# Optimization experiments

Hardware: AMD Instinct MI355X
Metric: run time of the kernel (lower is better)

The kernel has to match this reference:

```python
import jax, jax.numpy as jnp
import numpy as np

N = 50000
E = 800000
IN_DIM, HID, OUT = 128, 256, 256


def setup_inputs() -> dict:
    key = jax.random.key(0)
    ks = jax.random.split(key, 6)
    x = jax.random.normal(ks[0], (N, IN_DIM), dtype=jnp.float32)
    edge_index = jax.random.randint(ks[1], (2, E), 0, N, dtype=jnp.int64)
    W1 = jax.random.normal(ks[2], (IN_DIM, HID), dtype=jnp.float32) / np.sqrt(IN_DIM)
    b1 = jnp.zeros((HID,), dtype=jnp.float32)
    W2 = jax.random.normal(ks[3], (HID, OUT), dtype=jnp.float32) / np.sqrt(HID)
    b2 = jnp.zeros((OUT,), dtype=jnp.float32)
    return {"x": x, "edge_index": edge_index, "W1": W1, "b1": b1, "W2": W2, "b2": b2}


def _gcn_conv(x, edge_index, W, b):
    """PyG GCNConv: add self-loops, symmetric deg^-1/2 norm, linear, scatter-add, bias."""
    n = x.shape[0]
    loops = jnp.arange(n, dtype=edge_index.dtype)
    src = jnp.concatenate([edge_index[0], loops])  # [E+N]
    dst = jnp.concatenate([edge_index[1], loops])  # [E+N]
    deg = jax.ops.segment_sum(jnp.ones(src.shape[0], dtype=x.dtype), dst, num_segments=n)
    dinv = jnp.where(deg > 0, jax.lax.rsqrt(deg), jnp.zeros_like(deg))
    norm = dinv[src] * dinv[dst]  # [E+N]
    h = x @ W  # [N, out] small GEMM before gather (PyG order)
    msg = h[src] * norm[:, None]  # [E+N, out] -- dominant memory traffic
    out = jax.ops.segment_sum(msg, dst, num_segments=n)
    return out + b


def reference(x, edge_index, W1, b1, W2, b2):
    h = jax.nn.relu(_gcn_conv(x, edge_index, W1, b1))
    # dropout is identity in eval mode
    out = _gcn_conv(h, edge_index, W2, b2)
    # F.normalize(p=2, dim=-1, eps=1e-12)
    nrm = jnp.maximum(jnp.linalg.norm(out, axis=-1, keepdims=True), 1e-12)
    return out / nrm
```

## Files before the change

kernel.cpp:

```cpp
#include <hip/hip_runtime.h>
#include <hip/hip_bf16.h>


#define NNODE 50000
#define FDIM 256
#define SCAN_CHUNK 2048

typedef __attribute__((ext_vector_type(8))) short short8;
typedef __attribute__((ext_vector_type(4))) float f32x4;

__device__ __forceinline__ float bf2f(unsigned short u) {
    union { unsigned int i; float f; } c;
    c.i = ((unsigned int)u) << 16;
    return c.f;
}
__device__ __forceinline__ unsigned short f2bf(float f) {
    __hip_bfloat16 h = __float2bfloat16(f);
    return *reinterpret_cast<unsigned short*>(&h);
}

__global__ void count_kernel(const int* __restrict__ ei, int* __restrict__ counts, int E) {
    int e = blockIdx.x * blockDim.x + threadIdx.x;
    if (e < E) atomicAdd(&counts[ei[E + e]], 1);
}

__global__ __launch_bounds__(256) void scan_part1(const int* __restrict__ counts,
                                                  int* __restrict__ bsum, int n) {
    __shared__ int ws[4];
    int b = blockIdx.x, t = threadIdx.x;
    int base = b * SCAN_CHUNK + t * 8;
    int s = 0;
#pragma unroll
    for (int j = 0; j < 8; ++j) {
        int i = base + j;
        if (i < n) s += counts[i];
    }
#pragma unroll
    for (int off = 32; off >= 1; off >>= 1) s += __shfl_xor(s, off, 64);
    if ((t & 63) == 0) ws[t >> 6] = s;
    __syncthreads();
    if (t == 0) bsum[b] = ws[0] + ws[1] + ws[2] + ws[3];
}

__global__ void scan_part2(const int* __restrict__ bsum, int* __restrict__ boff,
                           int* __restrict__ row_ptr, int nb, int n) {
    int l = threadIdx.x;
    int v = (l < nb) ? bsum[l] : 0;
    int incl = v;
#pragma unroll
    for (int off = 1; off < 64; off <<= 1) {
        int u = __shfl_up(incl, off, 64);
        if (l >= off) incl += u;
    }
    if (l < nb) boff[l] = incl - v;
    if (l == nb - 1) row_ptr[n] = incl;
}

__global__ __launch_bounds__(256) void scan_part3(const int* __restrict__ counts,
                                                  const int* __restrict__ boff,
                                                  int* __restrict__ row_ptr,
                                                  int* __restrict__ cursor, int n) {
    __shared__ int ws[4];
    int b = blockIdx.x, t = threadIdx.x, lane = t & 63, wid = t >> 6;
    int base = b * SCAN_CHUNK + t * 8;
    int v[8];
    int s = 0;
#pragma unroll
    for (int j = 0; j < 8; ++j) {
        int i = base + j;
        v[j] = (i < n) ? counts[i] : 0;
        s += v[j];
    }
    int incl = s;
#pragma unroll
    for (int off = 1; off < 64; off <<= 1) {
        int u = __shfl_up(incl, off, 64);
        if (lane >= off) incl += u;
    }
    if (lane == 63) ws[wid] = incl;
    __syncthreads();
    int woff = 0;
    for (int u = 0; u < wid; ++u) woff += ws[u];
    int ex = boff[b] + woff + incl - s;
#pragma unroll
    for (int j = 0; j < 8; ++j) {
        int i = base + j;
        if (i < n) { row_ptr[i] = ex; cursor[i] = ex; }
        ex += v[j];
    }
}

__global__ void dinv_kernel(const int* __restrict__ counts, float* __restrict__ dinv, int n) {
    int i = blockIdx.x * blockDim.x + threadIdx.x;
    if (i < n) dinv[i] = rsqrtf((float)(counts[i] + 1));
}

__global__ void fill_kernel(const int* __restrict__ ei, const float* __restrict__ dinv,
                            int* __restrict__ cursor, int2* __restrict__ edata, int E) {
    int e = blockIdx.x * blockDim.x + threadIdx.x;
    if (e < E) {
        int s = ei[e];
        int d = ei[E + e];
        int pos = atomicAdd(&cursor[d], 1);
        float nm = dinv[s] * dinv[d];
        edata[pos] = make_int2(s, __float_as_int(nm));
    }
}

template <int K>
__global__ void wconv_kernel(const float* __restrict__ W, unsigned short* __restrict__ Wf) {
    int idx = blockIdx.x * blockDim.x + threadIdx.x;
    if (idx >= (K / 8) * 256) return;
    int g = idx >> 8, c = idx & 255;
    ushort4 lo = make_ushort4(f2bf(W[(8 * g + 0) * 256 + c]), f2bf(W[(8 * g + 1) * 256 + c]),
                              f2bf(W[(8 * g + 2) * 256 + c]), f2bf(W[(8 * g + 3) * 256 + c]));
    ushort4 hi = make_ushort4(f2bf(W[(8 * g + 4) * 256 + c]), f2bf(W[(8 * g + 5) * 256 + c]),
                              f2bf(W[(8 * g + 6) * 256 + c]), f2bf(W[(8 * g + 7) * 256 + c]));
    *reinterpret_cast<ushort4*>(&Wf[(size_t)idx * 8]) = lo;
    *reinterpret_cast<ushort4*>(&Wf[(size_t)idx * 8 + 4]) = hi;
}

template <int K, typename T>
__global__ __launch_bounds__(256) void gemm_mfma(const T* __restrict__ X,
                                                 const unsigned short* __restrict__ Wf,
                                                 unsigned short* __restrict__ H, int n) {
    __shared__ unsigned short As[(K / 8) * 32 * 8];
    int t = threadIdx.x;
    int row0 = blockIdx.x * 32;

    if constexpr (sizeof(T) == 4) {
#pragma unroll
        for (int i = 0; i < K / 32; ++i) {
            int o = 4 * (t + 256 * i);
            int row = o / K, k = o % K;
            int srow = row0 + row;
            float4 v = make_float4(0.f, 0.f, 0.f, 0.f);
            if (srow < n) v = *reinterpret_cast<const float4*>(&X[(size_t)srow * K + k]);
            ushort4 p = make_ushort4(f2bf(v.x), f2bf(v.y), f2bf(v.z), f2bf(v.w));
            int g = k >> 3;
            int idx = g * 32 + (row ^ (g & 7));
            *reinterpret_cast<ushort4*>(&As[idx * 8 + (k & 7)]) = p;
        }
    } else {
#pragma unroll
        for (int i = 0; i < K / 64; ++i) {
            int o = 8 * (t + 256 * i);
            int row = o / K, k = o % K;
            int srow = row0 + row;
            uint4 v = make_uint4(0u, 0u, 0u, 0u);
            if (srow < n) v = *reinterpret_cast<const uint4*>(&X[(size_t)srow * K + k]);
            int g = k >> 3;
            int idx = g * 32 + (row ^ (g & 7));
            *reinterpret_cast<uint4*>(&As[idx * 8]) = v;
        }
    }
    __syncthreads();

    int lane = t & 63, wv = t >> 6;
    int l15 = lane & 15, lhi = lane >> 4;
    f32x4 zero = {0.f, 0.f, 0.f, 0.f};
    f32x4 acc[2][4];
#pragma unroll
    for (int rf = 0; rf < 2; ++rf)
#pragma unroll
        for (int cf = 0; cf < 4; ++cf) acc[rf][cf] = zero;

#pragma unroll
    for (int s = 0; s < K / 32; ++s) {
        int g = 4 * s + lhi;
        int g7 = g & 7;
        short8 a0 = *reinterpret_cast<const short8*>(&As[(g * 32 + (l15 ^ g7)) * 8]);
        short8 a1 = *reinterpret_cast<const short8*>(&As[(g * 32 + ((16 + l15) ^ g7)) * 8]);
#pragma unroll
        for (int cf = 0; cf < 4; ++cf) {
            int col = 64 * wv + 16 * cf + l15;
            short8 b = *reinterpret_cast<const short8*>(&Wf[((size_t)g * 256 + col) * 8]);
            acc[0][cf] = __builtin_amdgcn_mfma_f32_16x16x32_bf16(a0, b, acc[0][cf], 0, 0, 0);
            acc[1][cf] = __builtin_amdgcn_mfma_f32_16x16x32_bf16(a1, b, acc[1][cf], 0, 0, 0);
        }
    }

#pragma unroll
    for (int rf = 0; rf < 2; ++rf)
#pragma unroll
        for (int cf = 0; cf < 4; ++cf) {
            f32x4 a = acc[rf][cf];
            int colb = 64 * wv + 16 * cf + l15;
#pragma unroll
            for (int j = 0; j < 4; ++j) {
                int row = row0 + 16 * rf + lhi * 4 + j;
                if (row < n) H[(size_t)row * 256 + colb] = f2bf(a[j]);
            }
        }
}

__device__ __forceinline__ void agg_core(const unsigned short* __restrict__ hb,
                                         const int* __restrict__ rowp,
                                         const int2* __restrict__ edata,
                                         const float* __restrict__ dinv,
                                         const float* __restrict__ bias,
                                         int node, int lane,
                                         float& a0, float& a1, float& a2, float& a3) {
    float di = dinv[node];
    float d2 = di * di;
    ushort4 sv = *(reinterpret_cast<const ushort4*>(hb + (size_t)node * FDIM) + lane);
    float4 bv = *(reinterpret_cast<const float4*>(bias) + lane);
    a0 = fmaf(bf2f(sv.x), d2, bv.x);
    a1 = fmaf(bf2f(sv.y), d2, bv.y);
    a2 = fmaf(bf2f(sv.z), d2, bv.z);
    a3 = fmaf(bf2f(sv.w), d2, bv.w);
    int beg = rowp[node], end = rowp[node + 1];
#pragma unroll 4
    for (int e = beg; e < end; ++e) {
        int2 ed = edata[e];
        float nm = __int_as_float(ed.y);
        ushort4 v = *(reinterpret_cast<const ushort4*>(hb + (size_t)ed.x * FDIM) + lane);
        a0 = fmaf(bf2f(v.x), nm, a0);
        a1 = fmaf(bf2f(v.y), nm, a1);
        a2 = fmaf(bf2f(v.z), nm, a2);
        a3 = fmaf(bf2f(v.w), nm, a3);
    }
}

__global__ __launch_bounds__(256) void agg_relu_kernel(const unsigned short* __restrict__ hb,
                                                       const int* __restrict__ rowp,
                                                       const int2* __restrict__ edata,
                                                       const float* __restrict__ dinv,
                                                       const float* __restrict__ bias,
                                                       unsigned short* __restrict__ outB, int n) {
    int node = (blockIdx.x * blockDim.x + threadIdx.x) >> 6;
    int lane = threadIdx.x & 63;
    if (node >= n) return;
    float a0, a1, a2, a3;
    agg_core(hb, rowp, edata, dinv, bias, node, lane, a0, a1, a2, a3);
    ushort4 o = make_ushort4(f2bf(fmaxf(a0, 0.f)), f2bf(fmaxf(a1, 0.f)),
                             f2bf(fmaxf(a2, 0.f)), f2bf(fmaxf(a3, 0.f)));
    *(reinterpret_cast<ushort4*>(outB + (size_t)node * FDIM) + lane) = o;
}

__global__ __launch_bounds__(256) void agg_norm_kernel(const unsigned short* __restrict__ hb,
                                                       const int* __restrict__ rowp,
                                                       const int2* __restrict__ edata,
                                                       const float* __restrict__ dinv,
                                                       const float* __restrict__ bias,
                                                       float* __restrict__ out, int n) {
    int node = (blockIdx.x * blockDim.x + threadIdx.x) >> 6;
    int lane = threadIdx.x & 63;
    if (node >= n) return;
    float a0, a1, a2, a3;
    agg_core(hb, rowp, edata, dinv, bias, node, lane, a0, a1, a2, a3);
    float ss = a0 * a0 + a1 * a1 + a2 * a2 + a3 * a3;
#pragma unroll
    for (int off = 32; off >= 1; off >>= 1) ss += __shfl_xor(ss, off, 64);
    float rinv = 1.f / fmaxf(sqrtf(ss), 1e-12f);
    float4 o = make_float4(a0 * rinv, a1 * rinv, a2 * rinv, a3 * rinv);
    *(reinterpret_cast<float4*>(out + (size_t)node * FDIM) + lane) = o;
}

extern "C" void kernel_launch(void* const* d_in, const int* in_sizes, int n_in,
                              void* d_out, int out_size, void* d_ws, size_t ws_size,
                              hipStream_t stream) {
    const float* x  = (const float*)d_in[0];
    const int*   ei = (const int*)d_in[1];
    const float* W1 = (const float*)d_in[2];
    const float* b1 = (const float*)d_in[3];
    const float* W2 = (const float*)d_in[4];
    const float* b2 = (const float*)d_in[5];
    float* out = (float*)d_out;

    const int N = NNODE;
    const int E = in_sizes[1] / 2;
    const int NB = (N + SCAN_CHUNK - 1) / SCAN_CHUNK;

    char* ws = (char*)d_ws;
    size_t off = 0;
    auto alloc = [&](size_t bytes) -> void* {
        void* p = ws + off;
        off = (off + bytes + 255) & ~(size_t)255;
        return p;
    };
    unsigned short* Hbf = (unsigned short*)alloc((size_t)N * FDIM * 2);
    unsigned short* Bbf = (unsigned short*)alloc((size_t)N * FDIM * 2);
    unsigned short* Wf1 = (unsigned short*)alloc((size_t)(128 / 8) * 256 * 8 * 2);
    unsigned short* Wf2 = (unsigned short*)alloc((size_t)(256 / 8) * 256 * 8 * 2);
    int*   counts = (int*)alloc((size_t)N * 4);
    int*   rowp   = (int*)alloc((size_t)(N + 1) * 4);
    int*   cursor = (int*)alloc((size_t)N * 4);
    float* dinv   = (float*)alloc((size_t)N * 4);
    int2*  edata  = (int2*)alloc((size_t)E * 8);
    int*   bsum   = (int*)alloc((size_t)NB * 4);
    int*   boff   = (int*)alloc((size_t)NB * 4);

    wconv_kernel<128><<<(16 * 256 + 255) / 256, 256, 0, stream>>>(W1, Wf1);
    wconv_kernel<256><<<(32 * 256 + 255) / 256, 256, 0, stream>>>(W2, Wf2);

    hipMemsetAsync(counts, 0, (size_t)N * 4, stream);
    count_kernel<<<(E + 255) / 256, 256, 0, stream>>>(ei, counts, E);
    scan_part1<<<NB, 256, 0, stream>>>(counts, bsum, N);
    scan_part2<<<1, 64, 0, stream>>>(bsum, boff, rowp, NB, N);
    scan_part3<<<NB, 256, 0, stream>>>(counts, boff, rowp, cursor, N);
    dinv_kernel<<<(N + 255) / 256, 256, 0, stream>>>(counts, dinv, N);
    fill_kernel<<<(E + 255) / 256, 256, 0, stream>>>(ei, dinv, cursor, edata, E);

    gemm_mfma<128, float><<<(N + 31) / 32, 256, 0, stream>>>(x, Wf1, Hbf, N);
    agg_relu_kernel<<<(N * 64 + 255) / 256, 256, 0, stream>>>(Hbf, rowp, edata, dinv, b1, Bbf, N);
    gemm_mfma<256, unsigned short><<<(N + 31) / 32, 256, 0, stream>>>(Bbf, Wf2, Hbf, N);
    agg_norm_kernel<<<(N * 64 + 255) / 256, 256, 0, stream>>>(Hbf, rowp, edata, dinv, b2, out, N);
}
```

Measured before the change: 254.1 us.

## Retile MFMA GEMM to 128x128 blocks with shared-memory weight tile

The GEMM moves from 32-row blocks that read weights straight from global memory to 128x128 output tiles on a 2D grid. Each block stages both the activation rows and a 128-column weight slice in LDS, using a row-based XOR swizzle. Each wave now computes a 64x64 sub-tile with 4x4 MFMAs, which raises operand reuse and cuts global weight reads. The final normalized output uses nontemporal stores. In exchange, LDS use per block rises a lot (up to 64KB+64KB for K=256), which may limit occupancy, and each row tile is loaded twice, once per column half.

```diff
diff --git a/kernel.cpp b/kernel.cpp
--- a/kernel.cpp
+++ b/kernel.cpp
@@ -124,72 +124,86 @@
 __global__ __launch_bounds__(256) void gemm_mfma(const T* __restrict__ X,
                                                  const unsigned short* __restrict__ Wf,
                                                  unsigned short* __restrict__ H, int n) {
-    __shared__ unsigned short As[(K / 8) * 32 * 8];
+    __shared__ unsigned short As[128 * K];
+    __shared__ unsigned short Bs[(K / 8) * 128 * 8];
     int t = threadIdx.x;
-    int row0 = blockIdx.x * 32;
+    int row0 = blockIdx.x * 128;
+    int cb = blockIdx.y;
 
     if constexpr (sizeof(T) == 4) {
 #pragma unroll
-        for (int i = 0; i < K / 32; ++i) {
+        for (int i = 0; i < (128 * K) / (4 * 256); ++i) {
             int o = 4 * (t + 256 * i);
             int row = o / K, k = o % K;
             int srow = row0 + row;
             float4 v = make_float4(0.f, 0.f, 0.f, 0.f);
             if (srow < n) v = *reinterpret_cast<const float4*>(&X[(size_t)srow * K + k]);
             ushort4 p = make_ushort4(f2bf(v.x), f2bf(v.y), f2bf(v.z), f2bf(v.w));
-            int g = k >> 3;
-            int idx = g * 32 + (row ^ (g & 7));
-            *reinterpret_cast<ushort4*>(&As[idx * 8 + (k & 7)]) = p;
+            int gx = (k >> 3) ^ (row & 7);
+            *reinterpret_cast<ushort4*>(&As[row * K + gx * 8 + (k & 7)]) = p;
         }
     } else {
 #pragma unroll
-        for (int i = 0; i < K / 64; ++i) {
+        for (int i = 0; i < (128 * K) / (8 * 256); ++i) {
             int o = 8 * (t + 256 * i);
             int row = o / K, k = o % K;
             int srow = row0 + row;
             uint4 v = make_uint4(0u, 0u, 0u, 0u);
             if (srow < n) v = *reinterpret_cast<const uint4*>(&X[(size_t)srow * K + k]);
-            int g = k >> 3;
-            int idx = g * 32 + (row ^ (g & 7));
-            *reinterpret_cast<uint4*>(&As[idx * 8]) = v;
-        }
+            int gx = (k >> 3) ^ (row & 7);
+            *reinterpret_cast<uint4*>(&As[row * K + gx * 8]) = v;
+        }
+    }
+#pragma unroll
+    for (int i = 0; i < ((K / 8) * 128) / 256; ++i) {
+        int idx = t + 256 * i;
+        int g = idx >> 7, c = idx & 127;
+        *reinterpret_cast<uint4*>(&Bs[idx * 8]) =
+            *reinterpret_cast<const uint4*>(&Wf[((size_t)g * 256 + cb * 128 + c) * 8]);
     }
     __syncthreads();
 
     int lane = t & 63, wv = t >> 6;
+    int rw = wv >> 1, cw = wv & 1;
     int l15 = lane & 15, lhi = lane >> 4;
     f32x4 zero = {0.f, 0.f, 0.f, 0.f};
-    f32x4 acc[2][4];
-#pragma unroll
-    for (int rf = 0; rf < 2; ++rf)
+    f32x4 acc[4][4];
+#pragma unroll
+    for (int rf = 0; rf < 4; ++rf)
 #pragma unroll
         for (int cf = 0; cf < 4; ++cf) acc[rf][cf] = zero;
 
 #pragma unroll
     for (int s = 0; s < K / 32; ++s) {
         int g = 4 * s + lhi;
-        int g7 = g & 7;
-        short8 a0 = *reinterpret_cast<const short8*>(&As[(g * 32 + (l15 ^ g7)) * 8]);
-        short8 a1 = *reinterpret_cast<const short8*>(&As[(g * 32 + ((16 + l15) ^ g7)) * 8]);
+        short8 a[4], b[4];
+#pragma unroll
+        for (int rf = 0; rf < 4; ++rf) {
+            int row = 64 * rw + 16 * rf + l15;
+            a[rf] = *reinterpret_cast<const short8*>(&As[row * K + (g ^ (row & 7)) * 8]);
+        }
 #pragma unroll
         for (int cf = 0; cf < 4; ++cf) {
-            int col = 64 * wv + 16 * cf + l15;
-            short8 b = *reinterpret_cast<const short8*>(&Wf[((size_t)g * 256 + col) * 8]);
-            acc[0][cf] = __builtin_amdgcn_mfma_f32_16x16x32_bf16(a0, b, acc[0][cf], 0, 0, 0);
-            acc[1][cf] = __builtin_amdgcn_mfma_f32_16x16x32_bf16(a1, b, acc[1][cf], 0, 0, 0);
-        }
-    }
-
-#pragma unroll
-    for (int rf = 0; rf < 2; ++rf)
+            int c = 64 * cw + 16 * cf + l15;
+            b[cf] = *reinterpret_cast<const short8*>(&Bs[(g * 128 + c) * 8]);
+        }
+#pragma unroll
+        for (int rf = 0; rf < 4; ++rf)
+#pragma unroll
+            for (int cf = 0; cf < 4; ++cf)
+                acc[rf][cf] = __builtin_amdgcn_mfma_f32_16x16x32_bf16(a[rf], b[cf], acc[rf][cf], 0, 0, 0);
+    }
+
+#pragma unroll
+    for (int rf = 0; rf < 4; ++rf)
 #pragma unroll
         for (int cf = 0; cf < 4; ++cf) {
             f32x4 a = acc[rf][cf];
-            int colb = 64 * wv + 16 * cf + l15;
+            int col = cb * 128 + 64 * cw + 16 * cf + l15;
 #pragma unroll
             for (int j = 0; j < 4; ++j) {
-                int row = row0 + 16 * rf + lhi * 4 + j;
-                if (row < n) H[(size_t)row * 256 + colb] = f2bf(a[j]);
+                int row = row0 + 64 * rw + 16 * rf + 4 * lhi + j;
+                if (row < n) H[(size_t)row * 256 + col] = f2bf(a[j]);
             }
         }
 }
@@ -253,8 +267,8 @@
 #pragma unroll
     for (int off = 32; off >= 1; off >>= 1) ss += __shfl_xor(ss, off, 64);
     float rinv = 1.f / fmaxf(sqrtf(ss), 1e-12f);
-    float4 o = make_float4(a0 * rinv, a1 * rinv, a2 * rinv, a3 * rinv);
-    *(reinterpret_cast<float4*>(out + (size_t)node * FDIM) + lane) = o;
+    f32x4 o = {a0 * rinv, a1 * rinv, a2 * rinv, a3 * rinv};
+    __builtin_nontemporal_store(o, reinterpret_cast<f32x4*>(out + (size_t)node * FDIM) + lane);
 }
 
 extern "C" void kernel_launch(void* const* d_in, const int* in_sizes, int n_in,
@@ -302,8 +316,9 @@
     dinv_kernel<<<(N + 255) / 256, 256, 0, stream>>>(counts, dinv, N);
     fill_kernel<<<(E + 255) / 256, 256, 0, stream>>>(ei, dinv, cursor, edata, E);
 
-    gemm_mfma<128, float><<<(N + 31) / 32, 256, 0, stream>>>(x, Wf1, Hbf, N);
+    dim3 ggrid((N + 127) / 128, 2);
+    gemm_mfma<128, float><<<ggrid, 256, 0, stream>>>(x, Wf1, Hbf, N);
     agg_relu_kernel<<<(N * 64 + 255) / 256, 256, 0, stream>>>(Hbf, rowp, edata, dinv, b1, Bbf, N);
-    gemm_mfma<256, unsigned short><<<(N + 31) / 32, 256, 0, stream>>>(Bbf, Wf2, Hbf, N);
+    gemm_mfma<256, unsigned short><<<ggrid, 256, 0, stream>>>(Bbf, Wf2, Hbf, N);
     agg_norm_kernel<<<(N * 64 + 255) / 256, 256, 0, stream>>>(Hbf, rowp, edata, dinv, b2, out, N);
 }
```

Measured after the change: 279.5 us. 1.1x slower.
